# Kernel tuning notes

Measured on AMD Instinct MI355X. Metric: run time of the kernel, lower is better.

## Reference

```python
import jax, jax.numpy as jnp
import numpy as np

N = 100000   # nodes
E = 3200000  # edges (avg degree 32)
F_IN = 128   # node feature dim (lazy in_channels)
C = 16       # GAT out_channels, heads=1
ED = 2       # edge_dim
B = 512      # graphs in batch
OUT_X = 64; OUT_Y = 64; ROT = 4
EPS = 1e-5


def _bn(x, g, b):
    # BatchNorm1d in training mode: biased batch variance, eps=1e-5
    mu = x.mean(0, keepdims=True)
    var = x.var(0, keepdims=True)
    return g * (x - mu) * jax.lax.rsqrt(var + EPS) + b


def _gat(x, src, dst, edge_attr, W, We, att_s, att_d, att_e, bias):
    # PyG GATConv, heads=1: self-loops added with fill_value='mean' edge attrs
    n = x.shape[0]
    deg = jax.ops.segment_sum(jnp.ones_like(dst, jnp.float32), dst, num_segments=n)
    loop_attr = jax.ops.segment_sum(edge_attr, dst, num_segments=n) / jnp.maximum(deg, 1.0)[:, None]
    idx = jnp.arange(n)
    src_f = jnp.concatenate([src, idx])
    dst_f = jnp.concatenate([dst, idx])
    ea = jnp.concatenate([edge_attr, loop_attr], axis=0)  # [E+N, ED]
    h = x @ W                      # [N, C]
    a_s = h @ att_s                # [N]
    a_d = h @ att_d                # [N]
    a_e = (ea @ We) @ att_e        # [E+N]
    logits = jax.nn.leaky_relu(a_s[src_f] + a_d[dst_f] + a_e, 0.2)
    m = jax.ops.segment_max(logits, dst_f, num_segments=n)  # every node has a self-loop
    ex = jnp.exp(logits - m[dst_f])
    alpha = ex / jax.ops.segment_sum(ex, dst_f, num_segments=n)[dst_f]
    return jax.ops.segment_sum(alpha[:, None] * h[src_f], dst_f, num_segments=n) + bias


def _glorot(k, shp):
    lim = float(np.sqrt(6.0 / (shp[0] + shp[1])))
    return jax.random.uniform(k, shp, jnp.float32, -lim, lim)


def setup_inputs() -> dict:
    key = jax.random.key(0)
    k = jax.random.split(key, 48)
    d = {}
    d['x'] = jax.random.normal(k[0], (N, F_IN), jnp.float32)
    d['edge_index'] = jax.random.randint(k[1], (2, E), 0, N)
    d['edge_attr'] = jax.random.normal(k[2], (E, ED), jnp.float32)
    d['batch'] = jnp.sort(jax.random.randint(k[3], (N,), 0, B))
    # gat1
    d['W1'] = _glorot(k[4], (F_IN, C)); d['We1'] = _glorot(k[5], (ED, C))
    d['as1'] = 0.1 * jax.random.normal(k[6], (C,)); d['ad1'] = 0.1 * jax.random.normal(k[7], (C,))
    d['ae1'] = 0.1 * jax.random.normal(k[8], (C,)); d['b1'] = jnp.zeros((C,), jnp.float32)
    # norm1 (BatchNorm on nodes)
    d['g1'] = 1.0 + 0.1 * jax.random.normal(k[9], (C,)); d['bb1'] = 0.1 * jax.random.normal(k[10], (C,))
    # gat2
    d['W2'] = _glorot(k[11], (C, C)); d['We2'] = _glorot(k[12], (ED, C))
    d['as2'] = 0.1 * jax.random.normal(k[13], (C,)); d['ad2'] = 0.1 * jax.random.normal(k[14], (C,))
    d['ae2'] = 0.1 * jax.random.normal(k[15], (C,)); d['b2'] = jnp.zeros((C,), jnp.float32)
    # D2RL MLP tail
    d['gL1'] = 1.0 + 0.1 * jax.random.normal(k[16], (C,)); d['bL1'] = 0.1 * jax.random.normal(k[17], (C,))
    d['Wl1'] = _glorot(k[18], (C, C)); d['bl1'] = 0.1 * jax.random.normal(k[19], (C,))
    d['gL2'] = 1.0 + 0.1 * jax.random.normal(k[20], (2 * C,)); d['bL2'] = 0.1 * jax.random.normal(k[21], (2 * C,))
    d['Wl2'] = _glorot(k[22], (2 * C, C)); d['bl2'] = 0.1 * jax.random.normal(k[23], (C,))
    d['gL3'] = 1.0 + 0.1 * jax.random.normal(k[24], (2 * C,)); d['bL3'] = 0.1 * jax.random.normal(k[25], (2 * C,))
    d['Wl3'] = _glorot(k[26], (2 * C, C)); d['bl3'] = 0.1 * jax.random.normal(k[27], (C,))
    d['Wx'] = _glorot(k[28], (C, OUT_X)); d['bx'] = 0.1 * jax.random.normal(k[29], (OUT_X,))
    d['Wy'] = _glorot(k[30], (C, OUT_Y)); d['by'] = 0.1 * jax.random.normal(k[31], (OUT_Y,))
    d['Wr'] = _glorot(k[32], (C, ROT)); d['br'] = 0.1 * jax.random.normal(k[33], (ROT,))
    return d


def reference(x, edge_index, edge_attr, batch,
              W1, We1, as1, ad1, ae1, b1, g1, bb1,
              W2, We2, as2, ad2, ae2, b2,
              gL1, bL1, Wl1, bl1, gL2, bL2, Wl2, bl2, gL3, bL3, Wl3, bl3,
              Wx, bx, Wy, by, Wr, br):
    src, dst = edge_index[0], edge_index[1]
    h = jax.nn.relu(_gat(x, src, dst, edge_attr, W1, We1, as1, ad1, ae1, b1))
    h = _bn(h, g1, bb1)
    h = jax.nn.relu(_gat(h, src, dst, edge_attr, W2, We2, as2, ad2, ae2, b2))
    # MeanAggregation over graphs
    cnt = jax.ops.segment_sum(jnp.ones((h.shape[0],), jnp.float32), batch, num_segments=B)
    xe = jax.ops.segment_sum(h, batch, num_segments=B) / jnp.maximum(cnt, 1.0)[:, None]  # [B, C]
    z = _bn(xe, gL1, bL1)
    z = jax.nn.relu(z @ Wl1 + bl1)
    z = _bn(jnp.concatenate([z, xe], axis=1), gL2, bL2)
    z = jax.nn.relu(z @ Wl2 + bl2)
    z = _bn(jnp.concatenate([z, xe], axis=1), gL3, bL3)
    z = jax.nn.relu(z @ Wl3 + bl3)
    xx = jax.nn.softmax(z @ Wx + bx, axis=1)
    y = jax.nn.softmax(z @ Wy + by, axis=1)
    rot = jax.nn.softmax(z @ Wr + br, axis=1)
    return (xx, y, rot)
```

## Files before the change

### kernel.cpp

```cpp
#include <hip/hip_runtime.h>
#include <hip/hip_fp16.h>
#include <math.h>

#define C 16
#define FIN 128

__global__ __launch_bounds__(256) void k_gemm1(
    const float* __restrict__ x, const float* __restrict__ W,
    const float* __restrict__ asw, const float* __restrict__ adw,
    float* __restrict__ h, float* __restrict__ a_s, float* __restrict__ a_d, int n) {
  __shared__ float xs[64 * 129];
  __shared__ float Ws[FIN * C];
  __shared__ float pAs[4][64], pAd[4][64];
  int t = threadIdx.x;
  int node0 = blockIdx.x * 64;
  for (int i = t; i < FIN * C; i += 256) Ws[i] = W[i];
  for (int i = t; i < 64 * FIN; i += 256) {
    int r = i >> 7, c = i & 127;
    int node = node0 + r;
    xs[r * 129 + c] = (node < n) ? x[(size_t)node * FIN + c] : 0.f;
  }
  __syncthreads();
  int nn = t & 63, cg = (t >> 6) * 4, grp = t >> 6;
  float a0 = 0.f, a1 = 0.f, a2 = 0.f, a3 = 0.f;
  const float* xr = &xs[nn * 129];
  #pragma unroll 8
  for (int k = 0; k < FIN; ++k) {
    float xv = xr[k];
    const float* wr = &Ws[k * C + cg];
    a0 += xv * wr[0]; a1 += xv * wr[1]; a2 += xv * wr[2]; a3 += xv * wr[3];
  }
  int node = node0 + nn;
  if (node < n) {
    float4* outp = (float4*)&h[(size_t)node * C + cg];
    *outp = make_float4(a0, a1, a2, a3);
  }
  pAs[grp][nn] = a0 * asw[cg] + a1 * asw[cg + 1] + a2 * asw[cg + 2] + a3 * asw[cg + 3];
  pAd[grp][nn] = a0 * adw[cg] + a1 * adw[cg + 1] + a2 * adw[cg + 2] + a3 * adw[cg + 3];
  __syncthreads();
  if (t < 64 && node0 + t < n) {
    a_s[node0 + t] = pAs[0][t] + pAs[1][t] + pAs[2][t] + pAs[3][t];
    a_d[node0 + t] = pAd[0][t] + pAd[1][t] + pAd[2][t] + pAd[3][t];
  }
}

__global__ __launch_bounds__(256) void k_hist_rank(
    const int* __restrict__ dst, int* __restrict__ counts,
    int* __restrict__ rank, int ne) {
  int e = blockIdx.x * 256 + threadIdx.x;
  if (e < ne) rank[e] = atomicAdd(&counts[dst[e]], 1);
}

__global__ __launch_bounds__(512) void k_scan1(const int* __restrict__ counts,
                                               int* __restrict__ bsum, int n) {
  __shared__ int sd[512];
  int i = blockIdx.x * 512 + threadIdx.x;
  sd[threadIdx.x] = (i < n) ? counts[i] : 0;
  __syncthreads();
  for (int s = 256; s > 0; s >>= 1) {
    if (threadIdx.x < s) sd[threadIdx.x] += sd[threadIdx.x + s];
    __syncthreads();
  }
  if (threadIdx.x == 0) bsum[blockIdx.x] = sd[0];
}

__global__ __launch_bounds__(512) void k_scan2(int* __restrict__ bsum,
                                               int* __restrict__ offs,
                                               int nblk, int n) {
  __shared__ int sd[512];
  int t = threadIdx.x;
  int v = (t < nblk) ? bsum[t] : 0;
  sd[t] = v;
  __syncthreads();
  for (int off = 1; off < 512; off <<= 1) {
    int x = (t >= off) ? sd[t - off] : 0;
    __syncthreads();
    sd[t] += x;
    __syncthreads();
  }
  if (t < nblk) bsum[t] = sd[t] - v;
  if (t == nblk - 1) offs[n] = sd[t];
}

__global__ __launch_bounds__(512) void k_scan3(const int* __restrict__ counts,
                                               const int* __restrict__ bsum,
                                               int* __restrict__ offs, int n) {
  __shared__ int sd[512];
  int t = threadIdx.x;
  int i = blockIdx.x * 512 + t;
  int v = (i < n) ? counts[i] : 0;
  sd[t] = v;
  __syncthreads();
  for (int off = 1; off < 512; off <<= 1) {
    int x = (t >= off) ? sd[t - off] : 0;
    __syncthreads();
    sd[t] += x;
    __syncthreads();
  }
  if (i < n) offs[i] = bsum[blockIdx.x] + sd[t] - v;
}

__global__ __launch_bounds__(256) void k_scatter(
    const int* __restrict__ src, const int* __restrict__ dst,
    const float2* __restrict__ ea, const int* __restrict__ offs,
    const int* __restrict__ rank, uint2* __restrict__ bucket, int ne) {
  int e = blockIdx.x * 256 + threadIdx.x;
  if (e >= ne) return;
  int d = dst[e];
  float2 a = ea[e];
  __half2 hh = __floats2half2_rn(a.x, a.y);
  unsigned int hb;
  memcpy(&hb, &hh, 4);
  bucket[offs[d] + rank[e]] = make_uint2((unsigned int)src[e], hb);
}

__global__ __launch_bounds__(256) void k_gather(
    const uint2* __restrict__ bucket, const int* __restrict__ offs,
    const float* __restrict__ a_s, const float* __restrict__ a_d,
    const float* __restrict__ h,
    const float* __restrict__ We, const float* __restrict__ aew,
    const float* __restrict__ bias,
    float* __restrict__ outv, float* __restrict__ bnsum, float* __restrict__ bnsq,
    int do_bn, int n) {
  __shared__ float sbn[32];
  int t = threadIdx.x;
  if (t < 32) sbn[t] = 0.f;
  __syncthreads();

  int node = blockIdx.x * 16 + (t >> 4);
  int l = t & 15;
  float we0 = 0.f, we1 = 0.f;
  #pragma unroll
  for (int c = 0; c < C; ++c) { we0 += We[c] * aew[c]; we1 += We[C + c] * aew[c]; }

  float acc[C];
  #pragma unroll
  for (int c = 0; c < C; ++c) acc[c] = 0.f;
  float den = 0.f, lax = 0.f, lay = 0.f;
  int o0 = 0, o1 = 0;
  float adi = 0.f, asi = 0.f;
  if (node < n) {
    o0 = offs[node]; o1 = offs[node + 1];
    adi = a_d[node]; asi = a_s[node];
    for (int e = o0 + l; e < o1; e += 16) {
      uint2 r = bucket[e];
      int s = (int)r.x;
      __half2 hh;
      memcpy(&hh, &r.y, 4);
      float2 eaf = __half22float2(hh);
      float lg = a_s[s] + adi + eaf.x * we0 + eaf.y * we1;
      lg = lg > 0.f ? lg : 0.2f * lg;
      float ex = __expf(lg);
      den += ex; lax += eaf.x; lay += eaf.y;
      const float4* hp = (const float4*)&h[(size_t)s * C];
      float4 h0 = hp[0], h1 = hp[1], h2 = hp[2], h3 = hp[3];
      acc[0] += ex * h0.x; acc[1] += ex * h0.y; acc[2] += ex * h0.z; acc[3] += ex * h0.w;
      acc[4] += ex * h1.x; acc[5] += ex * h1.y; acc[6] += ex * h1.z; acc[7] += ex * h1.w;
      acc[8] += ex * h2.x; acc[9] += ex * h2.y; acc[10] += ex * h2.z; acc[11] += ex * h2.w;
      acc[12] += ex * h3.x; acc[13] += ex * h3.y; acc[14] += ex * h3.z; acc[15] += ex * h3.w;
    }
  }
  #pragma unroll
  for (int off = 1; off < 16; off <<= 1) {
    den += __shfl_xor(den, off);
    lax += __shfl_xor(lax, off);
    lay += __shfl_xor(lay, off);
    #pragma unroll
    for (int c = 0; c < C; ++c) acc[c] += __shfl_xor(acc[c], off);
  }

  float v = 0.f;
  if (node < n) {
    float dgc = fmaxf((float)(o1 - o0), 1.f);
    float lg = asi + adi + (lax * we0 + lay * we1) / dgc;
    lg = lg > 0.f ? lg : 0.2f * lg;
    float ex = __expf(lg);
    float hi = h[(size_t)node * C + l];
    float tot = acc[l] + ex * hi;
    den += ex;
    v = fmaxf(tot / den + bias[l], 0.f);
    outv[(size_t)node * C + l] = v;
  }
  if (do_bn) {
    float s = v, q = v * v;
    s += __shfl_down(s, 32); s += __shfl_down(s, 16);
    q += __shfl_down(q, 32); q += __shfl_down(q, 16);
    if ((t & 63) < 16) {
      atomicAdd(&sbn[l], s);
      atomicAdd(&sbn[16 + l], q);
    }
    __syncthreads();
    if (t < 16) atomicAdd(&bnsum[t], sbn[t]);
    else if (t < 32) atomicAdd(&bnsq[t - 16], sbn[t]);
  }
}

__global__ void k_bnp(const float* __restrict__ bnsum, const float* __restrict__ bnsq,
                      const float* __restrict__ g, const float* __restrict__ bb,
                      float* __restrict__ scale, float* __restrict__ shift, float invn) {
  int c = threadIdx.x;
  if (c >= C) return;
  float mean = bnsum[c] * invn;
  float var = bnsq[c] * invn - mean * mean;
  float s = g[c] * rsqrtf(var + 1e-5f);
  scale[c] = s; shift[c] = bb[c] - mean * s;
}

__global__ __launch_bounds__(256) void k_node2(
    const float* __restrict__ outv, const float* __restrict__ scale,
    const float* __restrict__ shift, const float* __restrict__ W2,
    const float* __restrict__ asw, const float* __restrict__ adw,
    float* __restrict__ h, float* __restrict__ a_s, float* __restrict__ a_d, int n) {
  __shared__ float w2s[C * C];
  if (threadIdx.x < C * C) w2s[threadIdx.x] = W2[threadIdx.x];
  __syncthreads();
  int i = blockIdx.x * 256 + threadIdx.x;
  if (i >= n) return;
  float hn[C];
  #pragma unroll
  for (int c = 0; c < C; ++c) hn[c] = outv[(size_t)i * C + c] * scale[c] + shift[c];
  float h2[C];
  #pragma unroll
  for (int j = 0; j < C; ++j) {
    float acc = 0.f;
    #pragma unroll
    for (int c = 0; c < C; ++c) acc += hn[c] * w2s[c * C + j];
    h2[j] = acc;
  }
  float hs = 0.f, hd = 0.f;
  #pragma unroll
  for (int j = 0; j < C; ++j) { hs += h2[j] * asw[j]; hd += h2[j] * adw[j]; }
  a_s[i] = hs; a_d[i] = hd;
  float4* hp = (float4*)&h[(size_t)i * C];
  hp[0] = make_float4(h2[0], h2[1], h2[2], h2[3]);
  hp[1] = make_float4(h2[4], h2[5], h2[6], h2[7]);
  hp[2] = make_float4(h2[8], h2[9], h2[10], h2[11]);
  hp[3] = make_float4(h2[12], h2[13], h2[14], h2[15]);
}

__global__ void k_gstart(const int* __restrict__ batch, int* __restrict__ gs,
                         int n, int B_) {
  int g = blockIdx.x * blockDim.x + threadIdx.x;
  if (g > B_) return;
  if (g == B_) { gs[B_] = n; return; }
  int lo = 0, hi = n;
  while (lo < hi) { int mid = (lo + hi) >> 1; if (batch[mid] < g) lo = mid + 1; else hi = mid; }
  gs[g] = lo;
}

__global__ __launch_bounds__(256) void k_xe(
    const float* __restrict__ outv, const int* __restrict__ gs,
    float* __restrict__ xe, int B_) {
  int wave = blockIdx.x * 4 + (threadIdx.x >> 6);
  if (wave >= B_) return;
  int lane = threadIdx.x & 63;
  int c = lane & 15, sub = lane >> 4;
  int base = gs[wave], end = gs[wave + 1];
  float s = 0.f;
  for (int n0 = base + sub; n0 < end; n0 += 4) s += outv[(size_t)n0 * C + c];
  s += __shfl_down(s, 32);
  s += __shfl_down(s, 16);
  if (lane < 16) xe[(size_t)wave * C + c] = s / fmaxf((float)(end - base), 1.f);
}

__global__ __launch_bounds__(512) void k_tail_z3(
    const float* __restrict__ xe_in,
    const float* __restrict__ gL1, const float* __restrict__ bL1,
    const float* __restrict__ Wl1, const float* __restrict__ bl1,
    const float* __restrict__ gL2, const float* __restrict__ bL2,
    const float* __restrict__ Wl2, const float* __restrict__ bl2,
    const float* __restrict__ gL3, const float* __restrict__ bL3,
    const float* __restrict__ Wl3, const float* __restrict__ bl3,
    float* __restrict__ z3buf, int B_) {
  __shared__ float ssum[2 * C], ssq[2 * C], sc[2 * C], sh[2 * C];
  int t = threadIdx.x;
  float invB = 1.f / (float)B_;
  float xe[C];
  #pragma unroll
  for (int c = 0; c < C; ++c) xe[c] = xe_in[(size_t)t * C + c];

  if (t < 2 * C) { ssum[t] = 0.f; ssq[t] = 0.f; }
  __syncthreads();
  #pragma unroll
  for (int c = 0; c < C; ++c) {
    float s = xe[c], q = xe[c] * xe[c];
    for (int o = 32; o > 0; o >>= 1) { s += __shfl_down(s, o); q += __shfl_down(q, o); }
    if ((t & 63) == 0) { atomicAdd(&ssum[c], s); atomicAdd(&ssq[c], q); }
  }
  __syncthreads();
  if (t < C) {
    float mean = ssum[t] * invB, var = ssq[t] * invB - mean * mean;
    float s = gL1[t] * rsqrtf(var + 1e-5f);
    sc[t] = s; sh[t] = bL1[t] - mean * s;
  }
  __syncthreads();
  float z[C];
  #pragma unroll
  for (int j = 0; j < C; ++j) {
    float acc = bl1[j];
    #pragma unroll
    for (int c = 0; c < C; ++c) acc += (xe[c] * sc[c] + sh[c]) * Wl1[c * C + j];
    z[j] = fmaxf(acc, 0.f);
  }
  __syncthreads();

  if (t < 2 * C) { ssum[t] = 0.f; ssq[t] = 0.f; }
  __syncthreads();
  #pragma unroll
  for (int c = 0; c < C; ++c) {
    float s = z[c], q = z[c] * z[c];
    for (int o = 32; o > 0; o >>= 1) { s += __shfl_down(s, o); q += __shfl_down(q, o); }
    if ((t & 63) == 0) { atomicAdd(&ssum[c], s); atomicAdd(&ssq[c], q); }
    float s2 = xe[c], q2 = xe[c] * xe[c];
    for (int o = 32; o > 0; o >>= 1) { s2 += __shfl_down(s2, o); q2 += __shfl_down(q2, o); }
    if ((t & 63) == 0) { atomicAdd(&ssum[C + c], s2); atomicAdd(&ssq[C + c], q2); }
  }
  __syncthreads();
  if (t < 2 * C) {
    float mean = ssum[t] * invB, var = ssq[t] * invB - mean * mean;
    float s = gL2[t] * rsqrtf(var + 1e-5f);
    sc[t] = s; sh[t] = bL2[t] - mean * s;
  }
  __syncthreads();
  float z2[C];
  #pragma unroll
  for (int j = 0; j < C; ++j) {
    float acc = bl2[j];
    #pragma unroll
    for (int c = 0; c < C; ++c) acc += (z[c] * sc[c] + sh[c]) * Wl2[c * C + j];
    #pragma unroll
    for (int c = 0; c < C; ++c) acc += (xe[c] * sc[C + c] + sh[C + c]) * Wl2[(C + c) * C + j];
    z2[j] = fmaxf(acc, 0.f);
  }
  __syncthreads();

  if (t < 2 * C) { ssum[t] = 0.f; ssq[t] = 0.f; }
  __syncthreads();
  #pragma unroll
  for (int c = 0; c < C; ++c) {
    float s = z2[c], q = z2[c] * z2[c];
    for (int o = 32; o > 0; o >>= 1) { s += __shfl_down(s, o); q += __shfl_down(q, o); }
    if ((t & 63) == 0) { atomicAdd(&ssum[c], s); atomicAdd(&ssq[c], q); }
    float s2 = xe[c], q2 = xe[c] * xe[c];
    for (int o = 32; o > 0; o >>= 1) { s2 += __shfl_down(s2, o); q2 += __shfl_down(q2, o); }
    if ((t & 63) == 0) { atomicAdd(&ssum[C + c], s2); atomicAdd(&ssq[C + c], q2); }
  }
  __syncthreads();
  if (t < 2 * C) {
    float mean = ssum[t] * invB, var = ssq[t] * invB - mean * mean;
    float s = gL3[t] * rsqrtf(var + 1e-5f);
    sc[t] = s; sh[t] = bL3[t] - mean * s;
  }
  __syncthreads();
  #pragma unroll
  for (int j = 0; j < C; ++j) {
    float acc = bl3[j];
    #pragma unroll
    for (int c = 0; c < C; ++c) acc += (z2[c] * sc[c] + sh[c]) * Wl3[c * C + j];
    #pragma unroll
    for (int c = 0; c < C; ++c) acc += (xe[c] * sc[C + c] + sh[C + c]) * Wl3[(C + c) * C + j];
    z3buf[(size_t)t * C + j] = fmaxf(acc, 0.f);
  }
}

__global__ __launch_bounds__(256) void k_heads(
    const float* __restrict__ z3buf,
    const float* __restrict__ Wx, const float* __restrict__ bx,
    const float* __restrict__ Wy, const float* __restrict__ by,
    const float* __restrict__ Wr, const float* __restrict__ br,
    float* __restrict__ out, int B_) {
  int wv = blockIdx.x * 4 + (threadIdx.x >> 6);
  if (wv >= B_) return;
  int lane = threadIdx.x & 63;
  float z[C];
  #pragma unroll
  for (int c = 0; c < C; ++c) z[c] = z3buf[(size_t)wv * C + c];

  float ax = bx[lane];
  #pragma unroll
  for (int c = 0; c < C; ++c) ax += z[c] * Wx[c * 64 + lane];
  float m = ax;
  #pragma unroll
  for (int o = 32; o > 0; o >>= 1) m = fmaxf(m, __shfl_xor(m, o));
  float e = __expf(ax - m);
  float s = e;
  #pragma unroll
  for (int o = 32; o > 0; o >>= 1) s += __shfl_xor(s, o);
  out[(size_t)wv * 64 + lane] = e / s;

  float ay = by[lane];
  #pragma unroll
  for (int c = 0; c < C; ++c) ay += z[c] * Wy[c * 64 + lane];
  m = ay;
  #pragma unroll
  for (int o = 32; o > 0; o >>= 1) m = fmaxf(m, __shfl_xor(m, o));
  e = __expf(ay - m);
  s = e;
  #pragma unroll
  for (int o = 32; o > 0; o >>= 1) s += __shfl_xor(s, o);
  out[(size_t)B_ * 64 + (size_t)wv * 64 + lane] = e / s;

  if (lane < 4) {
    float ar = br[lane];
    #pragma unroll
    for (int c = 0; c < C; ++c) ar += z[c] * Wr[c * 4 + lane];
    float mr = ar;
    mr = fmaxf(mr, __shfl_xor(mr, 1));
    mr = fmaxf(mr, __shfl_xor(mr, 2));
    float er = __expf(ar - mr);
    float sr = er;
    sr += __shfl_xor(sr, 1);
    sr += __shfl_xor(sr, 2);
    out[(size_t)B_ * 128 + (size_t)wv * 4 + lane] = er / sr;
  }
}

extern "C" void kernel_launch(void* const* d_in, const int* in_sizes, int n_in,
                              void* d_out, int out_size, void* d_ws, size_t ws_size,
                              hipStream_t stream) {
  const float* x     = (const float*)d_in[0];
  const int*   eidx  = (const int*)d_in[1];
  const float* eattr = (const float*)d_in[2];
  const int*   batch = (const int*)d_in[3];
  const float* W1  = (const float*)d_in[4];
  const float* We1 = (const float*)d_in[5];
  const float* as1 = (const float*)d_in[6];
  const float* ad1 = (const float*)d_in[7];
  const float* ae1 = (const float*)d_in[8];
  const float* b1  = (const float*)d_in[9];
  const float* g1  = (const float*)d_in[10];
  const float* bb1 = (const float*)d_in[11];
  const float* W2  = (const float*)d_in[12];
  const float* We2 = (const float*)d_in[13];
  const float* as2 = (const float*)d_in[14];
  const float* ad2 = (const float*)d_in[15];
  const float* ae2 = (const float*)d_in[16];
  const float* b2  = (const float*)d_in[17];
  const float* gL1 = (const float*)d_in[18];
  const float* bL1 = (const float*)d_in[19];
  const float* Wl1 = (const float*)d_in[20];
  const float* bl1 = (const float*)d_in[21];
  const float* gL2 = (const float*)d_in[22];
  const float* bL2 = (const float*)d_in[23];
  const float* Wl2 = (const float*)d_in[24];
  const float* bl2 = (const float*)d_in[25];
  const float* gL3 = (const float*)d_in[26];
  const float* bL3 = (const float*)d_in[27];
  const float* Wl3 = (const float*)d_in[28];
  const float* bl3 = (const float*)d_in[29];
  const float* Wx  = (const float*)d_in[30];
  const float* bx  = (const float*)d_in[31];
  const float* Wy  = (const float*)d_in[32];
  const float* by  = (const float*)d_in[33];
  const float* Wr  = (const float*)d_in[34];
  const float* br  = (const float*)d_in[35];

  int N = in_sizes[3];
  int E = in_sizes[2] / 2;
  int B = out_size / 132;
  int nblk = (N + 511) / 512;

  char* w = (char*)d_ws;
  size_t o = 0;
  auto alloc = [&](size_t bytes) { char* p = w + o; o += (bytes + 15) & ~15ull; return p; };
  uint2* bucket  = (uint2*)alloc((size_t)E * 8);
  int*   rank    = (int*)alloc((size_t)E * 4);
  float* h       = (float*)alloc((size_t)N * C * 4);
  float* outv    = (float*)alloc((size_t)N * C * 4);
  float* a_s     = (float*)alloc((size_t)N * 4);
  float* a_d     = (float*)alloc((size_t)N * 4);
  int*   counts  = (int*)alloc((size_t)N * 4);
  int*   offs    = (int*)alloc((size_t)(N + 4) * 4);
  int*   bsum    = (int*)alloc((size_t)(nblk + 4) * 4);
  float* bn      = (float*)alloc(64 * 4);
  float* xe      = (float*)alloc((size_t)B * C * 4);
  int*   gs      = (int*)alloc((size_t)(B + 4) * 4);
  float* z3buf   = (float*)alloc((size_t)B * C * 4);

  const int* src = eidx;
  const int* dst = eidx + E;
  int ebl = (E + 255) / 256;
  int nbl = (N + 255) / 256;

  hipMemsetAsync(counts, 0, (size_t)N * 4, stream);
  hipMemsetAsync(bn, 0, 32 * 4, stream);

  k_gemm1<<<(N + 63) / 64, 256, 0, stream>>>(x, W1, as1, ad1, h, a_s, a_d, N);
  k_hist_rank<<<ebl, 256, 0, stream>>>(dst, counts, rank, E);
  k_scan1<<<nblk, 512, 0, stream>>>(counts, bsum, N);
  k_scan2<<<1, 512, 0, stream>>>(bsum, offs, nblk, N);
  k_scan3<<<nblk, 512, 0, stream>>>(counts, bsum, offs, N);
  k_scatter<<<ebl, 256, 0, stream>>>(src, dst, (const float2*)eattr, offs, rank, bucket, E);
  k_gather<<<(N + 15) / 16, 256, 0, stream>>>(bucket, offs, a_s, a_d, h, We1, ae1, b1,
                                              outv, bn, bn + 16, 1, N);
  k_bnp<<<1, 64, 0, stream>>>(bn, bn + 16, g1, bb1, bn + 32, bn + 48, 1.f / (float)N);
  k_node2<<<nbl, 256, 0, stream>>>(outv, bn + 32, bn + 48, W2, as2, ad2, h, a_s, a_d, N);
  k_gather<<<(N + 15) / 16, 256, 0, stream>>>(bucket, offs, a_s, a_d, h, We2, ae2, b2,
                                              outv, bn, bn + 16, 0, N);
  k_gstart<<<(B + 1 + 255) / 256, 256, 0, stream>>>(batch, gs, N, B);
  k_xe<<<(B + 3) / 4, 256, 0, stream>>>(outv, gs, xe, B);
  k_tail_z3<<<1, B, 0, stream>>>(xe, gL1, bL1, Wl1, bl1, gL2, bL2, Wl2, bl2,
                                 gL3, bL3, Wl3, bl3, z3buf, B);
  k_heads<<<(B + 3) / 4, 256, 0, stream>>>(z3buf, Wx, bx, Wy, by, Wr, br,
                                           (float*)d_out, B);
}
```

Measured before the change: 792.5 us.

## Split each h row across 4 lanes in GAT gather and recompute a_s

The gather kernel now has each node's 16-lane group process two edges per quad per step, with 4 lanes per edge each loading one float4 slice of the source h row. This replaces one lane loading the full 64-byte row. The per-edge a_s[s] gather is dropped: the source score is recomputed as a dot product of the h slice with att_s and reduced by two shuffles. This spreads the h gather across lanes and cuts the 16-accumulator register footprint and the long shuffle reduction, at the cost of extra shuffles and predicated second-edge loads.

Measured after the change: 771.2 us. -2.7%, faster.

```diff
diff --git a/kernel.cpp b/kernel.cpp
--- a/kernel.cpp
+++ b/kernel.cpp
@@ -119,7 +119,7 @@
     const float* __restrict__ a_s, const float* __restrict__ a_d,
     const float* __restrict__ h,
     const float* __restrict__ We, const float* __restrict__ aew,
-    const float* __restrict__ bias,
+    const float* __restrict__ asw, const float* __restrict__ bias,
     float* __restrict__ outv, float* __restrict__ bnsum, float* __restrict__ bnsq,
     int do_bn, int n) {
   __shared__ float sbn[32];
@@ -129,65 +129,93 @@
 
   int node = blockIdx.x * 16 + (t >> 4);
   int l = t & 15;
+  int q = l >> 2, f = l & 3;
+
   float we0 = 0.f, we1 = 0.f;
   #pragma unroll
   for (int c = 0; c < C; ++c) { we0 += We[c] * aew[c]; we1 += We[C + c] * aew[c]; }
-
-  float acc[C];
-  #pragma unroll
-  for (int c = 0; c < C; ++c) acc[c] = 0.f;
+  float4 aswf = ((const float4*)asw)[f];
+
+  float4 acc = make_float4(0.f, 0.f, 0.f, 0.f);
   float den = 0.f, lax = 0.f, lay = 0.f;
   int o0 = 0, o1 = 0;
   float adi = 0.f, asi = 0.f;
   if (node < n) {
     o0 = offs[node]; o1 = offs[node + 1];
     adi = a_d[node]; asi = a_s[node];
-    for (int e = o0 + l; e < o1; e += 16) {
-      uint2 r = bucket[e];
-      int s = (int)r.x;
-      __half2 hh;
-      memcpy(&hh, &r.y, 4);
-      float2 eaf = __half22float2(hh);
-      float lg = a_s[s] + adi + eaf.x * we0 + eaf.y * we1;
-      lg = lg > 0.f ? lg : 0.2f * lg;
-      float ex = __expf(lg);
-      den += ex; lax += eaf.x; lay += eaf.y;
-      const float4* hp = (const float4*)&h[(size_t)s * C];
-      float4 h0 = hp[0], h1 = hp[1], h2 = hp[2], h3 = hp[3];
-      acc[0] += ex * h0.x; acc[1] += ex * h0.y; acc[2] += ex * h0.z; acc[3] += ex * h0.w;
-      acc[4] += ex * h1.x; acc[5] += ex * h1.y; acc[6] += ex * h1.z; acc[7] += ex * h1.w;
-      acc[8] += ex * h2.x; acc[9] += ex * h2.y; acc[10] += ex * h2.z; acc[11] += ex * h2.w;
-      acc[12] += ex * h3.x; acc[13] += ex * h3.y; acc[14] += ex * h3.z; acc[15] += ex * h3.w;
+    for (int e = o0 + 2 * q; e < o1; e += 8) {
+      int e1 = e + 1;
+      bool p1 = e1 < o1;
+      uint2 r0 = bucket[e];
+      uint2 r1 = p1 ? bucket[e1] : make_uint2(0u, 0u);
+      float4 h0 = ((const float4*)(h + (size_t)r0.x * C))[f];
+      float4 h1 = p1 ? ((const float4*)(h + (size_t)r1.x * C))[f]
+                     : make_float4(0.f, 0.f, 0.f, 0.f);
+      __half2 hh0, hh1;
+      memcpy(&hh0, &r0.y, 4);
+      memcpy(&hh1, &r1.y, 4);
+      float2 ea0 = __half22float2(hh0);
+      float2 ea1 = __half22float2(hh1);
+      float d0 = h0.x * aswf.x + h0.y * aswf.y + h0.z * aswf.z + h0.w * aswf.w;
+      float d1 = h1.x * aswf.x + h1.y * aswf.y + h1.z * aswf.z + h1.w * aswf.w;
+      d0 += __shfl_xor(d0, 1); d0 += __shfl_xor(d0, 2);
+      d1 += __shfl_xor(d1, 1); d1 += __shfl_xor(d1, 2);
+      float lg0 = d0 + adi + ea0.x * we0 + ea0.y * we1;
+      float lg1 = d1 + adi + ea1.x * we0 + ea1.y * we1;
+      lg0 = lg0 > 0.f ? lg0 : 0.2f * lg0;
+      lg1 = lg1 > 0.f ? lg1 : 0.2f * lg1;
+      float ex0 = __expf(lg0);
+      float ex1 = p1 ? __expf(lg1) : 0.f;
+      den += ex0 + ex1;
+      lax += ea0.x + ea1.x;
+      lay += ea0.y + ea1.y;
+      acc.x += ex0 * h0.x + ex1 * h1.x;
+      acc.y += ex0 * h0.y + ex1 * h1.y;
+      acc.z += ex0 * h0.z + ex1 * h1.z;
+      acc.w += ex0 * h0.w + ex1 * h1.w;
     }
   }
-  #pragma unroll
-  for (int off = 1; off < 16; off <<= 1) {
-    den += __shfl_xor(den, off);
-    lax += __shfl_xor(lax, off);
-    lay += __shfl_xor(lay, off);
-    #pragma unroll
-    for (int c = 0; c < C; ++c) acc[c] += __shfl_xor(acc[c], off);
-  }
-
-  float v = 0.f;
+  acc.x += __shfl_xor(acc.x, 4); acc.y += __shfl_xor(acc.y, 4);
+  acc.z += __shfl_xor(acc.z, 4); acc.w += __shfl_xor(acc.w, 4);
+  den += __shfl_xor(den, 4); lax += __shfl_xor(lax, 4); lay += __shfl_xor(lay, 4);
+  acc.x += __shfl_xor(acc.x, 8); acc.y += __shfl_xor(acc.y, 8);
+  acc.z += __shfl_xor(acc.z, 8); acc.w += __shfl_xor(acc.w, 8);
+  den += __shfl_xor(den, 8); lax += __shfl_xor(lax, 8); lay += __shfl_xor(lay, 8);
+
+  float4 v = make_float4(0.f, 0.f, 0.f, 0.f);
   if (node < n) {
     float dgc = fmaxf((float)(o1 - o0), 1.f);
     float lg = asi + adi + (lax * we0 + lay * we1) / dgc;
     lg = lg > 0.f ? lg : 0.2f * lg;
-    float ex = __expf(lg);
-    float hi = h[(size_t)node * C + l];
-    float tot = acc[l] + ex * hi;
-    den += ex;
-    v = fmaxf(tot / den + bias[l], 0.f);
-    outv[(size_t)node * C + l] = v;
-  }
+    float exs = __expf(lg);
+    float4 hi = ((const float4*)(h + (size_t)node * C))[f];
+    float4 b4 = ((const float4*)bias)[f];
+    float dent = den + exs;
+    float inv = 1.f / dent;
+    v.x = fmaxf((acc.x + exs * hi.x) * inv + b4.x, 0.f);
+    v.y = fmaxf((acc.y + exs * hi.y) * inv + b4.y, 0.f);
+    v.z = fmaxf((acc.z + exs * hi.z) * inv + b4.z, 0.f);
+    v.w = fmaxf((acc.w + exs * hi.w) * inv + b4.w, 0.f);
+    if (q == 0) ((float4*)(outv + (size_t)node * C))[f] = v;
+  }
+
   if (do_bn) {
-    float s = v, q = v * v;
-    s += __shfl_down(s, 32); s += __shfl_down(s, 16);
-    q += __shfl_down(q, 32); q += __shfl_down(q, 16);
-    if ((t & 63) < 16) {
-      atomicAdd(&sbn[l], s);
-      atomicAdd(&sbn[16 + l], q);
+    float4 s4 = (node < n && q == 0) ? v : make_float4(0.f, 0.f, 0.f, 0.f);
+    float4 q4 = make_float4(s4.x * s4.x, s4.y * s4.y, s4.z * s4.z, s4.w * s4.w);
+    s4.x += __shfl_down(s4.x, 32); s4.y += __shfl_down(s4.y, 32);
+    s4.z += __shfl_down(s4.z, 32); s4.w += __shfl_down(s4.w, 32);
+    q4.x += __shfl_down(q4.x, 32); q4.y += __shfl_down(q4.y, 32);
+    q4.z += __shfl_down(q4.z, 32); q4.w += __shfl_down(q4.w, 32);
+    s4.x += __shfl_down(s4.x, 16); s4.y += __shfl_down(s4.y, 16);
+    s4.z += __shfl_down(s4.z, 16); s4.w += __shfl_down(s4.w, 16);
+    q4.x += __shfl_down(q4.x, 16); q4.y += __shfl_down(q4.y, 16);
+    q4.z += __shfl_down(q4.z, 16); q4.w += __shfl_down(q4.w, 16);
+    if ((t & 63) < 4) {
+      int c0 = f * 4;
+      atomicAdd(&sbn[c0 + 0], s4.x); atomicAdd(&sbn[c0 + 1], s4.y);
+      atomicAdd(&sbn[c0 + 2], s4.z); atomicAdd(&sbn[c0 + 3], s4.w);
+      atomicAdd(&sbn[16 + c0 + 0], q4.x); atomicAdd(&sbn[16 + c0 + 1], q4.y);
+      atomicAdd(&sbn[16 + c0 + 2], q4.z); atomicAdd(&sbn[16 + c0 + 3], q4.w);
     }
     __syncthreads();
     if (t < 16) atomicAdd(&bnsum[t], sbn[t]);
@@ -491,11 +519,11 @@
   k_scan2<<<1, 512, 0, stream>>>(bsum, offs, nblk, N);
   k_scan3<<<nblk, 512, 0, stream>>>(counts, bsum, offs, N);
   k_scatter<<<ebl, 256, 0, stream>>>(src, dst, (const float2*)eattr, offs, rank, bucket, E);
-  k_gather<<<(N + 15) / 16, 256, 0, stream>>>(bucket, offs, a_s, a_d, h, We1, ae1, b1,
+  k_gather<<<(N + 15) / 16, 256, 0, stream>>>(bucket, offs, a_s, a_d, h, We1, ae1, as1, b1,
                                               outv, bn, bn + 16, 1, N);
   k_bnp<<<1, 64, 0, stream>>>(bn, bn + 16, g1, bb1, bn + 32, bn + 48, 1.f / (float)N);
   k_node2<<<nbl, 256, 0, stream>>>(outv, bn + 32, bn + 48, W2, as2, ad2, h, a_s, a_d, N);
-  k_gather<<<(N + 15) / 16, 256, 0, stream>>>(bucket, offs, a_s, a_d, h, We2, ae2, b2,
+  k_gather<<<(N + 15) / 16, 256, 0, stream>>>(bucket, offs, a_s, a_d, h, We2, ae2, as2, b2,
                                               outv, bn, bn + 16, 0, N);
   k_gstart<<<(B + 1 + 255) / 256, 256, 0, stream>>>(batch, gs, N, B);
   k_xe<<<(B + 3) / 4, 256, 0, stream>>>(outv, gs, xe, B);
```

## Store node features in fp16, precompute edge logit terms, and split gather lanes

Applied to the files above, without the earlier changes.

Node features h are now stored in half precision, which halves the bytes moved by the random per-edge gathers. The scatter kernel now computes the per-edge attention scalar for both layers and packs the two values as half2 in the bucket, so the gather no longer recomputes them from raw edge attributes. The gather kernel uses 8 edge lanes times 2 feature halves with a one-ahead nontemporal prefetch of bucket entries, and writes its output as float4 vectors. In exchange, features and the edge logit terms lose precision, and the gather runs with fewer edge lanes per node.

Result: no change. 777.5 us (-1.9%).

```diff
diff --git a/kernel.cpp b/kernel.cpp
--- a/kernel.cpp
+++ b/kernel.cpp
@@ -5,10 +5,12 @@
 #define C 16
 #define FIN 128
 
+typedef unsigned int u32x2 __attribute__((ext_vector_type(2)));
+
 __global__ __launch_bounds__(256) void k_gemm1(
     const float* __restrict__ x, const float* __restrict__ W,
     const float* __restrict__ asw, const float* __restrict__ adw,
-    float* __restrict__ h, float* __restrict__ a_s, float* __restrict__ a_d, int n) {
+    __half* __restrict__ hh, float* __restrict__ a_s, float* __restrict__ a_d, int n) {
   __shared__ float xs[64 * 129];
   __shared__ float Ws[FIN * C];
   __shared__ float pAs[4][64], pAd[4][64];
@@ -32,8 +34,10 @@
   }
   int node = node0 + nn;
   if (node < n) {
-    float4* outp = (float4*)&h[(size_t)node * C + cg];
-    *outp = make_float4(a0, a1, a2, a3);
+    __half2 p0 = __floats2half2_rn(a0, a1), p1 = __floats2half2_rn(a2, a3);
+    unsigned u0, u1;
+    memcpy(&u0, &p0, 4); memcpy(&u1, &p1, 4);
+    *(uint2*)(hh + (size_t)node * 16 + cg) = make_uint2(u0, u1);
   }
   pAs[grp][nn] = a0 * asw[cg] + a1 * asw[cg + 1] + a2 * asw[cg + 2] + a3 * asw[cg + 3];
   pAd[grp][nn] = a0 * adw[cg] + a1 * adw[cg + 1] + a2 * adw[cg + 2] + a3 * adw[cg + 3];
@@ -103,91 +107,133 @@
 __global__ __launch_bounds__(256) void k_scatter(
     const int* __restrict__ src, const int* __restrict__ dst,
     const float2* __restrict__ ea, const int* __restrict__ offs,
-    const int* __restrict__ rank, uint2* __restrict__ bucket, int ne) {
+    const int* __restrict__ rank,
+    const float* __restrict__ We1, const float* __restrict__ ae1,
+    const float* __restrict__ We2, const float* __restrict__ ae2,
+    uint2* __restrict__ bucket, int ne) {
   int e = blockIdx.x * 256 + threadIdx.x;
   if (e >= ne) return;
+  float w01 = 0.f, w11 = 0.f, w02 = 0.f, w12 = 0.f;
+  #pragma unroll
+  for (int c = 0; c < C; ++c) {
+    w01 += We1[c] * ae1[c]; w11 += We1[C + c] * ae1[c];
+    w02 += We2[c] * ae2[c]; w12 += We2[C + c] * ae2[c];
+  }
   int d = dst[e];
   float2 a = ea[e];
-  __half2 hh = __floats2half2_rn(a.x, a.y);
-  unsigned int hb;
-  memcpy(&hb, &hh, 4);
-  bucket[offs[d] + rank[e]] = make_uint2((unsigned int)src[e], hb);
+  __half2 hp = __floats2half2_rn(a.x * w01 + a.y * w11, a.x * w02 + a.y * w12);
+  unsigned hb;
+  memcpy(&hb, &hp, 4);
+  bucket[offs[d] + rank[e]] = make_uint2((unsigned)src[e], hb);
 }
 
 __global__ __launch_bounds__(256) void k_gather(
     const uint2* __restrict__ bucket, const int* __restrict__ offs,
     const float* __restrict__ a_s, const float* __restrict__ a_d,
-    const float* __restrict__ h,
-    const float* __restrict__ We, const float* __restrict__ aew,
-    const float* __restrict__ bias,
+    const __half* __restrict__ hh, const float* __restrict__ bias,
     float* __restrict__ outv, float* __restrict__ bnsum, float* __restrict__ bnsq,
-    int do_bn, int n) {
+    int lay, int do_bn, int n) {
   __shared__ float sbn[32];
   int t = threadIdx.x;
   if (t < 32) sbn[t] = 0.f;
   __syncthreads();
 
   int node = blockIdx.x * 16 + (t >> 4);
-  int l = t & 15;
-  float we0 = 0.f, we1 = 0.f;
-  #pragma unroll
-  for (int c = 0; c < C; ++c) { we0 += We[c] * aew[c]; we1 += We[C + c] * aew[c]; }
-
-  float acc[C];
-  #pragma unroll
-  for (int c = 0; c < C; ++c) acc[c] = 0.f;
-  float den = 0.f, lax = 0.f, lay = 0.f;
+  int l = t & 15, f = l & 1, p = l >> 1;
+
+  float acc[8];
+  #pragma unroll
+  for (int j = 0; j < 8; ++j) acc[j] = 0.f;
+  float den = 0.f, ssum = 0.f;
   int o0 = 0, o1 = 0;
   float adi = 0.f, asi = 0.f;
   if (node < n) {
     o0 = offs[node]; o1 = offs[node + 1];
     adi = a_d[node]; asi = a_s[node];
-    for (int e = o0 + l; e < o1; e += 16) {
-      uint2 r = bucket[e];
+    int e = o0 + p;
+    u32x2 r = {0u, 0u};
+    if (e < o1) r = __builtin_nontemporal_load((const u32x2*)(bucket + e));
+    while (e < o1) {
+      int en = e + 8;
+      u32x2 rn = {0u, 0u};
+      if (en < o1) rn = __builtin_nontemporal_load((const u32x2*)(bucket + en));
       int s = (int)r.x;
-      __half2 hh;
-      memcpy(&hh, &r.y, 4);
-      float2 eaf = __half22float2(hh);
-      float lg = a_s[s] + adi + eaf.x * we0 + eaf.y * we1;
+      unsigned scb = r.y;
+      __half2 sc2;
+      memcpy(&sc2, &scb, 4);
+      float se = lay ? __high2float(sc2) : __low2float(sc2);
+      float asv = a_s[s];
+      uint4 hv = *(const uint4*)(hh + ((size_t)s << 4) + (f << 3));
+      float lg = asv + adi + se;
       lg = lg > 0.f ? lg : 0.2f * lg;
       float ex = __expf(lg);
-      den += ex; lax += eaf.x; lay += eaf.y;
-      const float4* hp = (const float4*)&h[(size_t)s * C];
-      float4 h0 = hp[0], h1 = hp[1], h2 = hp[2], h3 = hp[3];
-      acc[0] += ex * h0.x; acc[1] += ex * h0.y; acc[2] += ex * h0.z; acc[3] += ex * h0.w;
-      acc[4] += ex * h1.x; acc[5] += ex * h1.y; acc[6] += ex * h1.z; acc[7] += ex * h1.w;
-      acc[8] += ex * h2.x; acc[9] += ex * h2.y; acc[10] += ex * h2.z; acc[11] += ex * h2.w;
-      acc[12] += ex * h3.x; acc[13] += ex * h3.y; acc[14] += ex * h3.z; acc[15] += ex * h3.w;
+      den += ex; ssum += se;
+      __half2 t0, t1, t2, t3;
+      memcpy(&t0, &hv.x, 4); memcpy(&t1, &hv.y, 4);
+      memcpy(&t2, &hv.z, 4); memcpy(&t3, &hv.w, 4);
+      float2 g0 = __half22float2(t0), g1 = __half22float2(t1);
+      float2 g2 = __half22float2(t2), g3 = __half22float2(t3);
+      acc[0] += ex * g0.x; acc[1] += ex * g0.y;
+      acc[2] += ex * g1.x; acc[3] += ex * g1.y;
+      acc[4] += ex * g2.x; acc[5] += ex * g2.y;
+      acc[6] += ex * g3.x; acc[7] += ex * g3.y;
+      r = rn; e = en;
     }
   }
   #pragma unroll
-  for (int off = 1; off < 16; off <<= 1) {
+  for (int off = 2; off <= 8; off <<= 1) {
     den += __shfl_xor(den, off);
-    lax += __shfl_xor(lax, off);
-    lay += __shfl_xor(lay, off);
-    #pragma unroll
-    for (int c = 0; c < C; ++c) acc[c] += __shfl_xor(acc[c], off);
-  }
-
-  float v = 0.f;
+    ssum += __shfl_xor(ssum, off);
+    #pragma unroll
+    for (int j = 0; j < 8; ++j) acc[j] += __shfl_xor(acc[j], off);
+  }
+
+  float v[8];
+  #pragma unroll
+  for (int j = 0; j < 8; ++j) v[j] = 0.f;
   if (node < n) {
     float dgc = fmaxf((float)(o1 - o0), 1.f);
-    float lg = asi + adi + (lax * we0 + lay * we1) / dgc;
+    float lg = asi + adi + ssum / dgc;
     lg = lg > 0.f ? lg : 0.2f * lg;
-    float ex = __expf(lg);
-    float hi = h[(size_t)node * C + l];
-    float tot = acc[l] + ex * hi;
-    den += ex;
-    v = fmaxf(tot / den + bias[l], 0.f);
-    outv[(size_t)node * C + l] = v;
-  }
+    float exs = __expf(lg);
+    uint4 hv = *(const uint4*)(hh + ((size_t)node << 4) + (f << 3));
+    __half2 t0, t1, t2, t3;
+    memcpy(&t0, &hv.x, 4); memcpy(&t1, &hv.y, 4);
+    memcpy(&t2, &hv.z, 4); memcpy(&t3, &hv.w, 4);
+    float2 g0 = __half22float2(t0), g1 = __half22float2(t1);
+    float2 g2 = __half22float2(t2), g3 = __half22float2(t3);
+    float hs[8] = {g0.x, g0.y, g1.x, g1.y, g2.x, g2.y, g3.x, g3.y};
+    float inv = 1.f / (den + exs);
+    const float* bp = bias + f * 8;
+    #pragma unroll
+    for (int j = 0; j < 8; ++j)
+      v[j] = fmaxf((acc[j] + exs * hs[j]) * inv + bp[j], 0.f);
+    if (p == 0) {
+      float4* op = (float4*)(outv + ((size_t)node << 4));
+      op[f * 2]     = make_float4(v[0], v[1], v[2], v[3]);
+      op[f * 2 + 1] = make_float4(v[4], v[5], v[6], v[7]);
+    }
+  }
+
   if (do_bn) {
-    float s = v, q = v * v;
-    s += __shfl_down(s, 32); s += __shfl_down(s, 16);
-    q += __shfl_down(q, 32); q += __shfl_down(q, 16);
-    if ((t & 63) < 16) {
-      atomicAdd(&sbn[l], s);
-      atomicAdd(&sbn[16 + l], q);
+    float sv[8], qv[8];
+    bool act = (node < n) && (p == 0);
+    #pragma unroll
+    for (int j = 0; j < 8; ++j) {
+      sv[j] = act ? v[j] : 0.f;
+      qv[j] = sv[j] * sv[j];
+    }
+    #pragma unroll
+    for (int j = 0; j < 8; ++j) {
+      sv[j] += __shfl_down(sv[j], 32); qv[j] += __shfl_down(qv[j], 32);
+      sv[j] += __shfl_down(sv[j], 16); qv[j] += __shfl_down(qv[j], 16);
+    }
+    if ((t & 63) < 2) {
+      #pragma unroll
+      for (int j = 0; j < 8; ++j) {
+        atomicAdd(&sbn[f * 8 + j], sv[j]);
+        atomicAdd(&sbn[16 + f * 8 + j], qv[j]);
+      }
     }
     __syncthreads();
     if (t < 16) atomicAdd(&bnsum[t], sbn[t]);
@@ -210,7 +256,7 @@
     const float* __restrict__ outv, const float* __restrict__ scale,
     const float* __restrict__ shift, const float* __restrict__ W2,
     const float* __restrict__ asw, const float* __restrict__ adw,
-    float* __restrict__ h, float* __restrict__ a_s, float* __restrict__ a_d, int n) {
+    __half* __restrict__ hh, float* __restrict__ a_s, float* __restrict__ a_d, int n) {
   __shared__ float w2s[C * C];
   if (threadIdx.x < C * C) w2s[threadIdx.x] = W2[threadIdx.x];
   __syncthreads();
@@ -231,11 +277,15 @@
   #pragma unroll
   for (int j = 0; j < C; ++j) { hs += h2[j] * asw[j]; hd += h2[j] * adw[j]; }
   a_s[i] = hs; a_d[i] = hd;
-  float4* hp = (float4*)&h[(size_t)i * C];
-  hp[0] = make_float4(h2[0], h2[1], h2[2], h2[3]);
-  hp[1] = make_float4(h2[4], h2[5], h2[6], h2[7]);
-  hp[2] = make_float4(h2[8], h2[9], h2[10], h2[11]);
-  hp[3] = make_float4(h2[12], h2[13], h2[14], h2[15]);
+  unsigned wbits[8];
+  #pragma unroll
+  for (int j = 0; j < 8; ++j) {
+    __half2 hq = __floats2half2_rn(h2[2 * j], h2[2 * j + 1]);
+    memcpy(&wbits[j], &hq, 4);
+  }
+  uint4* hp = (uint4*)(hh + (size_t)i * 16);
+  hp[0] = make_uint4(wbits[0], wbits[1], wbits[2], wbits[3]);
+  hp[1] = make_uint4(wbits[4], wbits[5], wbits[6], wbits[7]);
 }
 
 __global__ void k_gstart(const int* __restrict__ batch, int* __restrict__ gs,
@@ -463,19 +513,19 @@
   char* w = (char*)d_ws;
   size_t o = 0;
   auto alloc = [&](size_t bytes) { char* p = w + o; o += (bytes + 15) & ~15ull; return p; };
-  uint2* bucket  = (uint2*)alloc((size_t)E * 8);
-  int*   rank    = (int*)alloc((size_t)E * 4);
-  float* h       = (float*)alloc((size_t)N * C * 4);
-  float* outv    = (float*)alloc((size_t)N * C * 4);
-  float* a_s     = (float*)alloc((size_t)N * 4);
-  float* a_d     = (float*)alloc((size_t)N * 4);
-  int*   counts  = (int*)alloc((size_t)N * 4);
-  int*   offs    = (int*)alloc((size_t)(N + 4) * 4);
-  int*   bsum    = (int*)alloc((size_t)(nblk + 4) * 4);
-  float* bn      = (float*)alloc(64 * 4);
-  float* xe      = (float*)alloc((size_t)B * C * 4);
-  int*   gs      = (int*)alloc((size_t)(B + 4) * 4);
-  float* z3buf   = (float*)alloc((size_t)B * C * 4);
+  uint2*  bucket = (uint2*)alloc((size_t)E * 8);
+  int*    rank   = (int*)alloc((size_t)E * 4);
+  __half* hh     = (__half*)alloc((size_t)N * C * 2);
+  float*  outv   = (float*)alloc((size_t)N * C * 4);
+  float*  a_s    = (float*)alloc((size_t)N * 4);
+  float*  a_d    = (float*)alloc((size_t)N * 4);
+  int*    counts = (int*)alloc((size_t)N * 4);
+  int*    offs   = (int*)alloc((size_t)(N + 4) * 4);
+  int*    bsum   = (int*)alloc((size_t)(nblk + 4) * 4);
+  float*  bn     = (float*)alloc(64 * 4);
+  float*  xe     = (float*)alloc((size_t)B * C * 4);
+  int*    gs     = (int*)alloc((size_t)(B + 4) * 4);
+  float*  z3buf  = (float*)alloc((size_t)B * C * 4);
 
   const int* src = eidx;
   const int* dst = eidx + E;
@@ -485,18 +535,19 @@
   hipMemsetAsync(counts, 0, (size_t)N * 4, stream);
   hipMemsetAsync(bn, 0, 32 * 4, stream);
 
-  k_gemm1<<<(N + 63) / 64, 256, 0, stream>>>(x, W1, as1, ad1, h, a_s, a_d, N);
+  k_gemm1<<<(N + 63) / 64, 256, 0, stream>>>(x, W1, as1, ad1, hh, a_s, a_d, N);
   k_hist_rank<<<ebl, 256, 0, stream>>>(dst, counts, rank, E);
   k_scan1<<<nblk, 512, 0, stream>>>(counts, bsum, N);
   k_scan2<<<1, 512, 0, stream>>>(bsum, offs, nblk, N);
   k_scan3<<<nblk, 512, 0, stream>>>(counts, bsum, offs, N);
-  k_scatter<<<ebl, 256, 0, stream>>>(src, dst, (const float2*)eattr, offs, rank, bucket, E);
-  k_gather<<<(N + 15) / 16, 256, 0, stream>>>(bucket, offs, a_s, a_d, h, We1, ae1, b1,
-                                              outv, bn, bn + 16, 1, N);
+  k_scatter<<<ebl, 256, 0, stream>>>(src, dst, (const float2*)eattr, offs, rank,
+                                     We1, ae1, We2, ae2, bucket, E);
+  k_gather<<<(N + 15) / 16, 256, 0, stream>>>(bucket, offs, a_s, a_d, hh, b1,
+                                              outv, bn, bn + 16, 0, 1, N);
   k_bnp<<<1, 64, 0, stream>>>(bn, bn + 16, g1, bb1, bn + 32, bn + 48, 1.f / (float)N);
-  k_node2<<<nbl, 256, 0, stream>>>(outv, bn + 32, bn + 48, W2, as2, ad2, h, a_s, a_d, N);
-  k_gather<<<(N + 15) / 16, 256, 0, stream>>>(bucket, offs, a_s, a_d, h, We2, ae2, b2,
-                                              outv, bn, bn + 16, 0, N);
+  k_node2<<<nbl, 256, 0, stream>>>(outv, bn + 32, bn + 48, W2, as2, ad2, hh, a_s, a_d, N);
+  k_gather<<<(N + 15) / 16, 256, 0, stream>>>(bucket, offs, a_s, a_d, hh, b2,
+                                              outv, bn, bn + 16, 1, 0, N);
   k_gstart<<<(B + 1 + 255) / 256, 256, 0, stream>>>(batch, gs, N, B);
   k_xe<<<(B + 3) / 4, 256, 0, stream>>>(outv, gs, xe, B);
   k_tail_z3<<<1, B, 0, stream>>>(xe, gL1, bL1, Wl1, bl1, gL2, bL2, Wl2, bl2,
```
